# Optimization experiments

Measured on AMD Instinct MI355X. Metric: run time of the kernel, lower is better.

Reference implementation:

```python
import jax, jax.numpy as jnp
import numpy as np

EMBED_DIM = 1024
NUM_HEADS = 16
HEAD_DIM = EMBED_DIM // NUM_HEADS
SCALE = HEAD_DIM ** -0.5


def setup_inputs() -> dict:
    key = jax.random.key(0)
    k1, k2, k3, k4 = jax.random.split(key, 4)
    B, N, C = 4, 2048, EMBED_DIM
    x = jax.random.normal(k1, (B, N, C), dtype=jnp.float32)
    # qkv: Linear(C, 3C, bias=False)
    w_qkv = jax.random.normal(k2, (3 * C, C), dtype=jnp.float32) * (C ** -0.5)
    # proj: Linear(C, C, bias=True)
    w_proj = jax.random.normal(k3, (C, C), dtype=jnp.float32) * (C ** -0.5)
    b_proj = jax.random.normal(k4, (C,), dtype=jnp.float32) * 0.01
    return {"x": x, "w_qkv": w_qkv, "w_proj": w_proj, "b_proj": b_proj}


def reference(x, w_qkv, w_proj, b_proj):
    B, N, C = x.shape
    H, D = NUM_HEADS, HEAD_DIM
    qkv = jnp.einsum('bnc,oc->bno', x, w_qkv)               # [B,N,3C]
    qkv = qkv.reshape(B, N, 3, H, D).transpose(2, 0, 3, 1, 4)  # [3,B,H,N,D]
    q, k, v = qkv[0], qkv[1], qkv[2]
    attn = jnp.einsum('bhnd,bhmd->bhnm', q, k) * SCALE       # [B,H,N,N]
    attn = jax.nn.softmax(attn, axis=-1)
    out = jnp.einsum('bhnm,bhmd->bhnd', attn, v)             # [B,H,N,D]
    out = out.transpose(0, 2, 1, 3).reshape(B, N, C)
    return jnp.einsum('bnc,oc->bno', out, w_proj) + b_proj
```

## Files before the change

kernel.cpp:

```cpp
#include <hip/hip_runtime.h>

#define B_ 4
#define N_ 2048
#define C_ 1024
#define H_ 16
#define D_ 64
#define M_ (B_*N_)

typedef _Float16 f16;
typedef __attribute__((ext_vector_type(2))) _Float16 f16x2;
typedef __attribute__((ext_vector_type(4))) _Float16 f16x4;
typedef __attribute__((ext_vector_type(8))) _Float16 f16x8;
typedef __attribute__((ext_vector_type(4))) float f32x4;
typedef __attribute__((ext_vector_type(16))) float f32x16;
typedef unsigned int u32;
typedef __attribute__((ext_vector_type(2))) u32 u32x2;
typedef __attribute__((ext_vector_type(4))) u32 u32x4;

__device__ __forceinline__ f32x4 mfma16(f16x8 a, f16x8 b, f32x4 c) {
  return __builtin_amdgcn_mfma_f32_16x16x32_f16(a, b, c, 0, 0, 0);
}
__device__ __forceinline__ f32x16 mfma32(f16x8 a, f16x8 b, f32x16 c) {
  return __builtin_amdgcn_mfma_f32_32x32x16_f16(a, b, c, 0, 0, 0);
}

__global__ void cast_f32_f16(const float* __restrict__ in, f16* __restrict__ out,
                             int n4, int scale_n4, float scale) {
  int i = blockIdx.x * blockDim.x + threadIdx.x;
  int stride = gridDim.x * blockDim.x;
  for (; i < n4; i += stride) {
    float4 v = reinterpret_cast<const float4*>(in)[i];
    float s = (i < scale_n4) ? scale : 1.0f;
    f16x4 o = { (f16)(v.x*s), (f16)(v.y*s), (f16)(v.z*s), (f16)(v.w*s) };
    reinterpret_cast<f16x4*>(out)[i] = o;
  }
}

template<int OUTMODE>
__global__ __launch_bounds__(512, 1) void gemm_p(
    const f16* __restrict__ A, const f16* __restrict__ Bm,
    f16* __restrict__ outH, float* __restrict__ outF,
    const float* __restrict__ bias, f16* __restrict__ vt, int Nn, int K, int nsup)
{
  __shared__ __align__(16) f16 As[3][128*64];
  __shared__ __align__(16) f16 Bs[3][256*64];
  const int tid = threadIdx.x;
  const int lane = tid & 63, wid = tid >> 6;
  const int wm = wid >> 2, wn = wid & 3;
  const int g = lane >> 4, r15 = lane & 15;
  const int rmod = r15 & 3;
  const int gx = (g ^ rmod) * 8;

  const int s = blockIdx.x >> 4, w16 = blockIdx.x & 15;
  const int s_swz = (s & 7) * (2 * nsup) + (s >> 3);
  const int sm = s_swz / nsup, sn = s_swz % nsup;
  const int m0 = (sm * 4 + (w16 >> 2)) * 128;
  const int n0 = (sn * 4 + (w16 & 3)) * 256;

  const int arow = tid >> 2, aslot = tid & 3;
  const int akc = aslot ^ (arow & 3);
  const f16* abase  = A  + (size_t)(m0 + arow) * K + akc * 8;
  const f16* bbase0 = Bm + (size_t)(n0 + arow) * K + akc * 8;
  const f16* bbase1 = Bm + (size_t)(n0 + arow + 128) * K + akc * 8;

  #define STAGE(buf, kofs, kh)                                                        \
    do {                                                                              \
      __builtin_amdgcn_global_load_lds(                                               \
        (const __attribute__((address_space(1))) u32*)(abase + (kofs) + (kh)*32),     \
        (__attribute__((address_space(3))) u32*)&As[buf][(kh)*4096 + tid*8], 16,0,0); \
      __builtin_amdgcn_global_load_lds(                                               \
        (const __attribute__((address_space(1))) u32*)(bbase0 + (kofs) + (kh)*32),    \
        (__attribute__((address_space(3))) u32*)&Bs[buf][(kh)*8192 + tid*8], 16,0,0); \
      __builtin_amdgcn_global_load_lds(                                               \
        (const __attribute__((address_space(1))) u32*)(bbase1 + (kofs) + (kh)*32),    \
        (__attribute__((address_space(3))) u32*)&Bs[buf][(kh)*8192 + (tid+512)*8], 16,0,0); \
    } while (0)

  f32x4 acc[4][4] = {};
  const int nt = K / 64;

  STAGE(0, 0, 0); STAGE(0, 0, 1);
  STAGE(1, 64, 0); STAGE(1, 64, 1);
  asm volatile("s_waitcnt vmcnt(6)" ::: "memory");
  __builtin_amdgcn_s_barrier();

  for (int t = 0; t < nt; ++t) {
    const int bc = t % 3;
    const int bn = (t + 2) % 3;
#pragma unroll
    for (int kk = 0; kk < 2; ++kk) {
      f16x8 af[4], bf[4];
#pragma unroll
      for (int m = 0; m < 4; ++m)
        af[m] = *reinterpret_cast<const f16x8*>(&As[bc][kk*4096 + (wm*64 + m*16 + r15)*32 + gx]);
#pragma unroll
      for (int n = 0; n < 4; ++n)
        bf[n] = *reinterpret_cast<const f16x8*>(&Bs[bc][kk*8192 + (wn*64 + n*16 + r15)*32 + gx]);
      if (t + 2 < nt) STAGE(bn, (t + 2) * 64, kk);
      __builtin_amdgcn_sched_barrier(0);
      __builtin_amdgcn_s_barrier();
      asm volatile("s_waitcnt lgkmcnt(0)" ::: "memory");
      __builtin_amdgcn_sched_barrier(0);
      __builtin_amdgcn_s_setprio(1);
#pragma unroll
      for (int m = 0; m < 4; ++m)
#pragma unroll
        for (int n = 0; n < 4; ++n)
          acc[m][n] = mfma16(af[m], bf[n], acc[m][n]);
      __builtin_amdgcn_s_setprio(0);
      if (kk == 1) {
        if (t + 2 < nt)      asm volatile("s_waitcnt vmcnt(6)" ::: "memory");
        else if (t + 1 < nt) asm volatile("s_waitcnt vmcnt(0)" ::: "memory");
      }
      __builtin_amdgcn_s_barrier();
    }
  }
  #undef STAGE

  if (OUTMODE == 0 && n0 >= 2*C_) {
    const int b = m0 >> 11;
    const int rbase = (m0 - b*2048) + wm*64 + g*4;
#pragma unroll
    for (int m = 0; m < 4; ++m) {
#pragma unroll
      for (int n = 0; n < 4; ++n) {
        int cv = (n0 - 2*C_) + wn*64 + n*16 + r15;
        f16x4 o;
#pragma unroll
        for (int r = 0; r < 4; ++r) o[r] = (f16)acc[m][n][r];
        *reinterpret_cast<f16x4*>(
            vt + (((size_t)(b*1024 + cv)) << 11) + rbase + m*16) = o;
      }
    }
  } else {
#pragma unroll
    for (int m = 0; m < 4; ++m) {
#pragma unroll
      for (int n = 0; n < 4; ++n) {
#pragma unroll
        for (int r = 0; r < 4; ++r) {
          int row = m0 + wm*64 + m*16 + g*4 + r;
          int col = n0 + wn*64 + n*16 + r15;
          if (OUTMODE == 0) {
            outH[(size_t)row * Nn + col] = (f16)acc[m][n][r];
          } else {
            outF[(size_t)row * Nn + col] = acc[m][n][r] + bias[col];
          }
        }
      }
    }
  }
}

__global__ __launch_bounds__(256, 4) void attn_kernel(
    const f16* __restrict__ qkv, const f16* __restrict__ vt,
    f16* __restrict__ attn_out)
{
  __shared__ __align__(16) f16 Ks[2][64*64];
  __shared__ __align__(16) f16 Vs[2][64*64];
  const int tid = threadIdx.x;
  const int lane = tid & 63, w = tid >> 6;
  const int hi = lane >> 5;
  const int r31 = lane & 31;
  const int rm = r31 & 7;
  const int blk = blockIdx.x;
  const int xcd = blk & 7, idx = blk >> 3;
  const int bh = xcd + 8 * (idx >> 4);
  const int bx = idx & 15;
  const int b = bh >> 4, h = bh & 15;
  const int q0 = bx * 128 + w * 32;
  const int RS = 3 * C_;

  f16x8 qf[4];
  {
    const f16* qrow = qkv + (size_t)(b*N_ + q0 + r31) * RS + h*D_;
#pragma unroll
    for (int kk = 0; kk < 4; ++kk)
      qf[kk] = *reinterpret_cast<const f16x8*>(qrow + kk*16 + hi*8);
  }

  f32x16 acc0 = {}, acc1 = {};
  const f16x2 one2 = { (f16)1.0f, (f16)1.0f };
  float la = 0.f, lb = 0.f;

  int cc0 = w*64 + lane, cc1 = 256 + w*64 + lane;
  int R0 = cc0 >> 3, s0_ = (cc0 & 7) ^ (R0 & 7);
  int R1 = cc1 >> 3, s1_ = (cc1 & 7) ^ (R1 & 7);
  const f16* kg0 = qkv + (size_t)(b*N_ + R0) * RS + C_ + h*D_ + s0_*8;
  const f16* kg1 = qkv + (size_t)(b*N_ + R1) * RS + C_ + h*D_ + s1_*8;
  const f16* vg0 = vt + (size_t)(bh*D_ + R0) * N_ + s0_*8;
  const f16* vg1 = vt + (size_t)(bh*D_ + R1) * N_ + s1_*8;

  auto stage = [&](int bufi, int kv0) {
    __builtin_amdgcn_global_load_lds(
      (const __attribute__((address_space(1))) u32*)(kg0 + (size_t)kv0 * RS),
      (__attribute__((address_space(3))) u32*)&Ks[bufi][(w*64)*8], 16, 0, 0);
    __builtin_amdgcn_global_load_lds(
      (const __attribute__((address_space(1))) u32*)(kg1 + (size_t)kv0 * RS),
      (__attribute__((address_space(3))) u32*)&Ks[bufi][(256 + w*64)*8], 16, 0, 0);
    __builtin_amdgcn_global_load_lds(
      (const __attribute__((address_space(1))) u32*)(vg0 + kv0),
      (__attribute__((address_space(3))) u32*)&Vs[bufi][(w*64)*8], 16, 0, 0);
    __builtin_amdgcn_global_load_lds(
      (const __attribute__((address_space(1))) u32*)(vg1 + kv0),
      (__attribute__((address_space(3))) u32*)&Vs[bufi][(256 + w*64)*8], 16, 0, 0);
  };

  int cur = 0;
  stage(0, 0);
  __syncthreads();

  for (int it = 0; it < N_/64; ++it) {
    if (it + 1 < N_/64) stage(cur ^ 1, (it + 1) * 64);
    const f16* KsC = Ks[cur];
    const f16* VsC = Vs[cur];

#pragma unroll
    for (int hh = 0; hh < 2; ++hh) {
      f32x16 T;
      {
        const f32x16 Zc = {};
        __builtin_amdgcn_s_setprio(1);
        int ch = ((hi ^ rm) << 3);
        f16x8 k0 = *reinterpret_cast<const f16x8*>(&KsC[(hh*32 + r31)*64 + ch]);
        T = mfma32(k0, qf[0], Zc);
#pragma unroll
        for (int kk = 1; kk < 4; ++kk) {
          int ch2 = (((kk*2 + hi) ^ rm) << 3);
          f16x8 kx = *reinterpret_cast<const f16x8*>(&KsC[(hh*32 + r31)*64 + ch2]);
          T = mfma32(kx, qf[kk], T);
        }
        __builtin_amdgcn_s_setprio(0);
      }

#pragma unroll
      for (int c2 = 0; c2 < 2; ++c2) {
        float p0 = __builtin_amdgcn_exp2f(T[8*c2 + 0]);
        float p1 = __builtin_amdgcn_exp2f(T[8*c2 + 1]);
        float p2 = __builtin_amdgcn_exp2f(T[8*c2 + 2]);
        float p3 = __builtin_amdgcn_exp2f(T[8*c2 + 3]);
        float p4 = __builtin_amdgcn_exp2f(T[8*c2 + 4]);
        float p5 = __builtin_amdgcn_exp2f(T[8*c2 + 5]);
        float p6 = __builtin_amdgcn_exp2f(T[8*c2 + 6]);
        float p7 = __builtin_amdgcn_exp2f(T[8*c2 + 7]);
        u32 w0 = __builtin_bit_cast(u32, __builtin_amdgcn_cvt_pkrtz(p0, p1));
        u32 w1 = __builtin_bit_cast(u32, __builtin_amdgcn_cvt_pkrtz(p2, p3));
        u32 w2 = __builtin_bit_cast(u32, __builtin_amdgcn_cvt_pkrtz(p4, p5));
        u32 w3 = __builtin_bit_cast(u32, __builtin_amdgcn_cvt_pkrtz(p6, p7));
        la = __builtin_amdgcn_fdot2(__builtin_bit_cast(f16x2, w0), one2, la, false);
        lb = __builtin_amdgcn_fdot2(__builtin_bit_cast(f16x2, w1), one2, lb, false);
        la = __builtin_amdgcn_fdot2(__builtin_bit_cast(f16x2, w2), one2, la, false);
        lb = __builtin_amdgcn_fdot2(__builtin_bit_cast(f16x2, w3), one2, lb, false);

        u32x2 r02 = __builtin_amdgcn_permlane32_swap(w0, w2, false, false);
        u32x2 r13 = __builtin_amdgcn_permlane32_swap(w1, w3, false, false);
        u32x4 fw = { r02[0], r13[0], r02[1], r13[1] };
        f16x8 pf = __builtin_bit_cast(f16x8, fw);

        int c = hh*2 + c2;
        int ch = (((c*2 + hi) ^ rm) << 3);
        f16x8 v0 = *reinterpret_cast<const f16x8*>(&VsC[r31*64 + ch]);
        f16x8 v1 = *reinterpret_cast<const f16x8*>(&VsC[(32 + r31)*64 + ch]);
        __builtin_amdgcn_s_setprio(1);
        acc0 = mfma32(v0, pf, acc0);
        acc1 = mfma32(v1, pf, acc1);
        __builtin_amdgcn_s_setprio(0);
      }
    }

    __syncthreads();
    cur ^= 1;
  }

  float l_own = la + lb;
  float l = l_own + __shfl_xor(l_own, 32);
  float inv = 1.0f / l;
  f16* orow = attn_out + (size_t)(b*N_ + q0 + r31) * C_ + h*D_;
#pragma unroll
  for (int g2 = 0; g2 < 4; ++g2) {
    f16x4 o0, o1;
#pragma unroll
    for (int j = 0; j < 4; ++j) {
      o0[j] = (f16)(acc0[g2*4 + j] * inv);
      o1[j] = (f16)(acc1[g2*4 + j] * inv);
    }
    *reinterpret_cast<f16x4*>(orow + g2*8 + hi*4)      = o0;
    *reinterpret_cast<f16x4*>(orow + 32 + g2*8 + hi*4) = o1;
  }
}

extern "C" void kernel_launch(void* const* d_in, const int* in_sizes, int n_in,
                              void* d_out, int out_size, void* d_ws, size_t ws_size,
                              hipStream_t stream) {
  const float* x      = (const float*)d_in[0];
  const float* w_qkv  = (const float*)d_in[1];
  const float* w_proj = (const float*)d_in[2];
  const float* b_proj = (const float*)d_in[3];
  float* out = (float*)d_out;

  char* ws = (char*)d_ws;
  f16* xb     = (f16*)(ws);
  f16* wqkvb  = (f16*)(ws + 16777216);
  f16* wprojb = (f16*)(ws + 23068672);
  f16* qkvb   = (f16*)(ws + 25165824);
  f16* vtb    = (f16*)(ws + 75497472);
  f16* attnb  = xb;

  cast_f32_f16<<<2048, 256, 0, stream>>>(x,      xb,     (M_*C_)/4, 0, 1.0f);
  cast_f32_f16<<<1024, 256, 0, stream>>>(w_qkv,  wqkvb,  (3*C_*C_)/4, (C_*C_)/4, 0.18033688011112042f);
  cast_f32_f16<<<512,  256, 0, stream>>>(w_proj, wprojb, (C_*C_)/4, 0, 1.0f);

  gemm_p<0><<<dim3(768), 512, 0, stream>>>(
      xb, wqkvb, qkvb, nullptr, nullptr, vtb, 3*C_, C_, 3);

  attn_kernel<<<dim3(1024), 256, 0, stream>>>(qkvb, vtb, attnb);

  gemm_p<1><<<dim3(256), 512, 0, stream>>>(
      attnb, wprojb, nullptr, out, b_proj, nullptr, C_, C_, 1);
}
```

Measured before the change: 213.1 us.

## Shrink GEMM tiles to 128x128 with 256 threads and fuse cast kernels

The three f32-to-f16 cast launches become one kernel that walks all three buffers. The GEMM tile shrinks from 128x256 with 8 waves to 128x128 with 4 waves, and each K-step drops to 32. Launch bounds now allow 3 blocks per CU and the grids double, aiming for higher occupancy and better load balance. In exchange, each loaded byte is reused less and more barriers are hit per unit of K.

Result: faster. 194.2 us (median of 4 runs) (-8.8%).

```diff
diff --git a/kernel.cpp b/kernel.cpp
--- a/kernel.cpp
+++ b/kernel.cpp
@@ -24,96 +24,107 @@
   return __builtin_amdgcn_mfma_f32_32x32x16_f16(a, b, c, 0, 0, 0);
 }
 
-__global__ void cast_f32_f16(const float* __restrict__ in, f16* __restrict__ out,
-                             int n4, int scale_n4, float scale) {
+#define XN4   ((M_*C_)/4)
+#define WQN4  ((3*C_*C_)/4)
+#define WPN4  ((C_*C_)/4)
+__global__ void cast_all(const float* __restrict__ x, const float* __restrict__ wqkv,
+                         const float* __restrict__ wproj,
+                         f16* __restrict__ xb, f16* __restrict__ wqkvb,
+                         f16* __restrict__ wprojb) {
+  const float qs = 0.18033688011112042f;
   int i = blockIdx.x * blockDim.x + threadIdx.x;
   int stride = gridDim.x * blockDim.x;
-  for (; i < n4; i += stride) {
-    float4 v = reinterpret_cast<const float4*>(in)[i];
-    float s = (i < scale_n4) ? scale : 1.0f;
+  for (; i < XN4 + WQN4 + WPN4; i += stride) {
+    const float* src; f16* dst; int j; float s = 1.0f;
+    if (i < XN4) { src = x; dst = xb; j = i; }
+    else if (i < XN4 + WQN4) {
+      src = wqkv; dst = wqkvb; j = i - XN4;
+      if (j < (C_*C_)/4) s = qs;
+    } else { src = wproj; dst = wprojb; j = i - XN4 - WQN4; }
+    float4 v = reinterpret_cast<const float4*>(src)[j];
     f16x4 o = { (f16)(v.x*s), (f16)(v.y*s), (f16)(v.z*s), (f16)(v.w*s) };
-    reinterpret_cast<f16x4*>(out)[i] = o;
+    reinterpret_cast<f16x4*>(dst)[j] = o;
   }
 }
 
 template<int OUTMODE>
-__global__ __launch_bounds__(512, 1) void gemm_p(
+__global__ __launch_bounds__(256, 3) void gemm_p(
     const f16* __restrict__ A, const f16* __restrict__ Bm,
     f16* __restrict__ outH, float* __restrict__ outF,
-    const float* __restrict__ bias, f16* __restrict__ vt, int Nn, int K, int nsup)
+    const float* __restrict__ bias, f16* __restrict__ vt, int Nn, int K, int nsupn)
 {
-  __shared__ __align__(16) f16 As[3][128*64];
-  __shared__ __align__(16) f16 Bs[3][256*64];
+  __shared__ __align__(16) f16 As[3][128*32];
+  __shared__ __align__(16) f16 Bs[3][128*32];
   const int tid = threadIdx.x;
   const int lane = tid & 63, wid = tid >> 6;
-  const int wm = wid >> 2, wn = wid & 3;
+  const int wm = wid >> 1, wn = wid & 1;
   const int g = lane >> 4, r15 = lane & 15;
   const int rmod = r15 & 3;
   const int gx = (g ^ rmod) * 8;
 
   const int s = blockIdx.x >> 4, w16 = blockIdx.x & 15;
-  const int s_swz = (s & 7) * (2 * nsup) + (s >> 3);
-  const int sm = s_swz / nsup, sn = s_swz % nsup;
+  const int cpx = (gridDim.x >> 4) >> 3;
+  const int s_swz = (s & 7) * cpx + (s >> 3);
+  const int sm = s_swz / nsupn, sn = s_swz % nsupn;
   const int m0 = (sm * 4 + (w16 >> 2)) * 128;
-  const int n0 = (sn * 4 + (w16 & 3)) * 256;
+  const int n0 = (sn * 4 + (w16 & 3)) * 128;
 
   const int arow = tid >> 2, aslot = tid & 3;
   const int akc = aslot ^ (arow & 3);
   const f16* abase  = A  + (size_t)(m0 + arow) * K + akc * 8;
-  const f16* bbase0 = Bm + (size_t)(n0 + arow) * K + akc * 8;
-  const f16* bbase1 = Bm + (size_t)(n0 + arow + 128) * K + akc * 8;
-
-  #define STAGE(buf, kofs, kh)                                                        \
+  const f16* abase2 = A  + (size_t)(m0 + arow + 64) * K + akc * 8;
+  const f16* bbase  = Bm + (size_t)(n0 + arow) * K + akc * 8;
+  const f16* bbase2 = Bm + (size_t)(n0 + arow + 64) * K + akc * 8;
+
+  #define STAGE(buf, kofs)                                                            \
     do {                                                                              \
       __builtin_amdgcn_global_load_lds(                                               \
-        (const __attribute__((address_space(1))) u32*)(abase + (kofs) + (kh)*32),     \
-        (__attribute__((address_space(3))) u32*)&As[buf][(kh)*4096 + tid*8], 16,0,0); \
+        (const __attribute__((address_space(1))) u32*)(abase + (kofs)),               \
+        (__attribute__((address_space(3))) u32*)&As[buf][tid*8], 16, 0, 0);           \
       __builtin_amdgcn_global_load_lds(                                               \
-        (const __attribute__((address_space(1))) u32*)(bbase0 + (kofs) + (kh)*32),    \
-        (__attribute__((address_space(3))) u32*)&Bs[buf][(kh)*8192 + tid*8], 16,0,0); \
+        (const __attribute__((address_space(1))) u32*)(abase2 + (kofs)),              \
+        (__attribute__((address_space(3))) u32*)&As[buf][(tid+256)*8], 16, 0, 0);     \
       __builtin_amdgcn_global_load_lds(                                               \
-        (const __attribute__((address_space(1))) u32*)(bbase1 + (kofs) + (kh)*32),    \
-        (__attribute__((address_space(3))) u32*)&Bs[buf][(kh)*8192 + (tid+512)*8], 16,0,0); \
+        (const __attribute__((address_space(1))) u32*)(bbase + (kofs)),               \
+        (__attribute__((address_space(3))) u32*)&Bs[buf][tid*8], 16, 0, 0);           \
+      __builtin_amdgcn_global_load_lds(                                               \
+        (const __attribute__((address_space(1))) u32*)(bbase2 + (kofs)),              \
+        (__attribute__((address_space(3))) u32*)&Bs[buf][(tid+256)*8], 16, 0, 0);     \
     } while (0)
 
   f32x4 acc[4][4] = {};
-  const int nt = K / 64;
-
-  STAGE(0, 0, 0); STAGE(0, 0, 1);
-  STAGE(1, 64, 0); STAGE(1, 64, 1);
-  asm volatile("s_waitcnt vmcnt(6)" ::: "memory");
+  const int nt = K / 32;
+
+  STAGE(0, 0);
+  STAGE(1, 32);
+  asm volatile("s_waitcnt vmcnt(4)" ::: "memory");
   __builtin_amdgcn_s_barrier();
 
   for (int t = 0; t < nt; ++t) {
     const int bc = t % 3;
     const int bn = (t + 2) % 3;
-#pragma unroll
-    for (int kk = 0; kk < 2; ++kk) {
-      f16x8 af[4], bf[4];
-#pragma unroll
-      for (int m = 0; m < 4; ++m)
-        af[m] = *reinterpret_cast<const f16x8*>(&As[bc][kk*4096 + (wm*64 + m*16 + r15)*32 + gx]);
+    f16x8 af[4], bf[4];
+#pragma unroll
+    for (int m = 0; m < 4; ++m)
+      af[m] = *reinterpret_cast<const f16x8*>(&As[bc][(wm*64 + m*16 + r15)*32 + gx]);
+#pragma unroll
+    for (int n = 0; n < 4; ++n)
+      bf[n] = *reinterpret_cast<const f16x8*>(&Bs[bc][(wn*64 + n*16 + r15)*32 + gx]);
+    if (t + 2 < nt) STAGE(bn, (t + 2) * 32);
+    __builtin_amdgcn_sched_barrier(0);
+    __builtin_amdgcn_s_barrier();
+    asm volatile("s_waitcnt lgkmcnt(0)" ::: "memory");
+    __builtin_amdgcn_sched_barrier(0);
+    __builtin_amdgcn_s_setprio(1);
+#pragma unroll
+    for (int m = 0; m < 4; ++m)
 #pragma unroll
       for (int n = 0; n < 4; ++n)
-        bf[n] = *reinterpret_cast<const f16x8*>(&Bs[bc][kk*8192 + (wn*64 + n*16 + r15)*32 + gx]);
-      if (t + 2 < nt) STAGE(bn, (t + 2) * 64, kk);
-      __builtin_amdgcn_sched_barrier(0);
-      __builtin_amdgcn_s_barrier();
-      asm volatile("s_waitcnt lgkmcnt(0)" ::: "memory");
-      __builtin_amdgcn_sched_barrier(0);
-      __builtin_amdgcn_s_setprio(1);
-#pragma unroll
-      for (int m = 0; m < 4; ++m)
-#pragma unroll
-        for (int n = 0; n < 4; ++n)
-          acc[m][n] = mfma16(af[m], bf[n], acc[m][n]);
-      __builtin_amdgcn_s_setprio(0);
-      if (kk == 1) {
-        if (t + 2 < nt)      asm volatile("s_waitcnt vmcnt(6)" ::: "memory");
-        else if (t + 1 < nt) asm volatile("s_waitcnt vmcnt(0)" ::: "memory");
-      }
-      __builtin_amdgcn_s_barrier();
-    }
+        acc[m][n] = mfma16(af[m], bf[n], acc[m][n]);
+    __builtin_amdgcn_s_setprio(0);
+    if (t + 2 < nt)      asm volatile("s_waitcnt vmcnt(4)" ::: "memory");
+    else if (t + 1 < nt) asm volatile("s_waitcnt vmcnt(0)" ::: "memory");
+    __builtin_amdgcn_s_barrier();
   }
   #undef STAGE
 
@@ -306,15 +317,13 @@
   f16* vtb    = (f16*)(ws + 75497472);
   f16* attnb  = xb;
 
-  cast_f32_f16<<<2048, 256, 0, stream>>>(x,      xb,     (M_*C_)/4, 0, 1.0f);
-  cast_f32_f16<<<1024, 256, 0, stream>>>(w_qkv,  wqkvb,  (3*C_*C_)/4, (C_*C_)/4, 0.18033688011112042f);
-  cast_f32_f16<<<512,  256, 0, stream>>>(w_proj, wprojb, (C_*C_)/4, 0, 1.0f);
-
-  gemm_p<0><<<dim3(768), 512, 0, stream>>>(
-      xb, wqkvb, qkvb, nullptr, nullptr, vtb, 3*C_, C_, 3);
+  cast_all<<<2048, 256, 0, stream>>>(x, w_qkv, w_proj, xb, wqkvb, wprojb);
+
+  gemm_p<0><<<dim3(1536), 256, 0, stream>>>(
+      xb, wqkvb, qkvb, nullptr, nullptr, vtb, 3*C_, C_, 6);
 
   attn_kernel<<<dim3(1024), 256, 0, stream>>>(qkvb, vtb, attnb);
 
-  gemm_p<1><<<dim3(256), 512, 0, stream>>>(
-      attnb, wprojb, nullptr, out, b_proj, nullptr, C_, C_, 1);
-}
+  gemm_p<1><<<dim3(512), 256, 0, stream>>>(
+      attnb, wprojb, nullptr, out, b_proj, nullptr, C_, C_, 2);
+}
```
